# Optimization experiments

Measured on AMD Instinct MI355X. Metric: run time of the kernel, lower is better.

The kernel has to match this reference:

```python
import jax, jax.numpy as jnp
import numpy as np
import math
from math import factorial
from fractions import Fraction

LMAX = 2
N_ATOMS = 30000
N_FEAT = 128


def _cg(j1, m1, j2, m2, j3, m3):
    # Clebsch-Gordan coefficient <j1 m1 j2 m2 | j3 m3> (Racah formula, exact rationals)
    if m3 != m1 + m2 or j3 < abs(j1 - j2) or j3 > j1 + j2:
        return 0.0
    f = factorial
    pref = Fraction((2 * j3 + 1) * f(j3 + j1 - j2) * f(j3 - j1 + j2) * f(j1 + j2 - j3), f(j1 + j2 + j3 + 1))
    pref *= f(j3 + m3) * f(j3 - m3) * f(j1 - m1) * f(j1 + m1) * f(j2 - m2) * f(j2 + m2)
    s = Fraction(0)
    kmin = max(0, j2 - j3 - m1, j1 - j3 + m2)
    kmax = min(j1 + j2 - j3, j1 - m1, j2 + m2)
    for k in range(kmin, kmax + 1):
        s += Fraction((-1) ** k, f(k) * f(j1 + j2 - j3 - k) * f(j1 - m1 - k) * f(j2 + m2 - k) * f(j3 - j2 + m1 + k) * f(j3 - j1 - m2 + k))
    return math.sqrt(float(pref)) * float(s)


def _sh_indices(lmax):
    lidx = np.concatenate([np.full(2 * l + 1, l) for l in range(lmax + 1)])
    midx = np.concatenate([np.arange(-l, l + 1) for l in range(lmax + 1)])
    return lidx, midx


def _build_sparse_cg(lmax):
    # dense complex-SH CG tensor over combined (l,m) index s, size S=(lmax+1)^2
    lidx, midx = _sh_indices(lmax)
    S = len(lidx)
    cg = np.zeros((S, S, S))
    for a in range(S):
        for b in range(S):
            for c in range(S):
                cg[a, b, c] = _cg(int(lidx[a]), int(midx[a]), int(lidx[b]), int(midx[b]), int(lidx[c]), int(midx[c]))
    # unitary complex SH -> real SH transform (rows: real, cols: complex)
    m1 = midx[:, None]
    m2 = midx[None, :]
    U = ((m1 == 0) & (m2 == 0)) * (1.0 + 0.0j)
    U = U + ((m1 > 0) & (m2 > 0) & (m1 == m2)) * ((-1.0) ** m1 / math.sqrt(2))
    U = U + ((m1 > 0) & (m2 < 0) & (m1 == -m2)) * (1.0 / math.sqrt(2))
    U = U + ((m1 < 0) & (m2 > 0) & (m1 == -m2)) * (-1.0j * (-1.0) ** m1 / math.sqrt(2))
    U = U + ((m1 < 0) & (m2 < 0) & (m1 == m2)) * (1.0j / math.sqrt(2))
    U = U * (lidx[:, None] == lidx[None, :])
    cg_rsh = np.einsum('ijk,mi,nj,ok->mno', cg.astype(np.complex128), U, U, U.conj())
    # parity invariance mask
    parity = (-1.0) ** lidx
    pmask = (parity[:, None, None] * parity[None, :, None]) == parity[None, None, :]
    cg_real = (cg_rsh * pmask).real
    # sparsify (threshold kills complex-arithmetic residues ~1e-17)
    i1, i2, io = np.nonzero(np.abs(cg_real) > 1e-12)
    return cg_real[i1, i2, io].astype(np.float32), i1.astype(np.int32), i2.astype(np.int32), io.astype(np.int32)


def setup_inputs() -> dict:
    key = jax.random.key(0)
    k1, k2 = jax.random.split(key)
    S = (LMAX + 1) ** 2
    cg_sparse, i1, i2, io = _build_sparse_cg(LMAX)
    return {
        'x1': jax.random.normal(k1, (N_ATOMS, S, N_FEAT), dtype=jnp.float32),
        'x2': jax.random.normal(k2, (N_ATOMS, S, N_FEAT), dtype=jnp.float32),
        'cg_sparse': jnp.asarray(cg_sparse),
        'idx_in_1': jnp.asarray(i1),
        'idx_in_2': jnp.asarray(i2),
        'idx_out': jnp.asarray(io),
    }


def reference(x1, x2, cg_sparse, idx_in_1, idx_in_2, idx_out):
    S = (LMAX + 1) ** 2
    # gather paths [n_atoms, P, F], multiply by sparse CG, scatter-add over output (l,m)
    y = x1[:, idx_in_1, :] * x2[:, idx_in_2, :] * cg_sparse[None, :, None]
    out = jnp.zeros((x1.shape[0], S, x1.shape[2]), x1.dtype).at[:, idx_out, :].add(y)
    return out
```

## Files before the change

### kernel.cpp

```cpp
#include <hip/hip_runtime.h>


#define NS 9
#define NF 128
#define NF4 32

constexpr int LQ[9] = {0, 1, 1, 1, 2, 2, 2, 2, 2};
constexpr int MQ[9] = {0, -1, 0, 1, -2, -1, 0, 1, 2};

constexpr bool cg_compat(int A, int B, int O) {
  const int l1 = LQ[A], l2 = LQ[B], l3 = LQ[O];
  const int m1 = MQ[A], m2 = MQ[B], m3 = MQ[O];
  const int lo = (l1 > l2) ? (l1 - l2) : (l2 - l1);
  if (l3 < lo || l3 > l1 + l2) return false;
  if ((l1 + l2 + l3) & 1) return false;
  const int u = (m1 < 0) ? -m1 : m1;
  const int v = (m2 < 0) ? -m2 : m2;
  const int w = (m3 < 0) ? -m3 : m3;
  const int d = (u > v) ? (u - v) : (v - u);
  if (!(w == u + v || w == d)) return false;
  const bool mixed = (m1 < 0) != (m2 < 0);
  if (mixed != (m3 < 0)) return false;
  return true;
}

__global__ void build_dense_cg(const float* __restrict__ cg,
                               const int* __restrict__ i1,
                               const int* __restrict__ i2,
                               const int* __restrict__ io,
                               int nnz, float* __restrict__ C) {
  const int t = threadIdx.x;
  for (int i = t; i < NS * NS * NS; i += blockDim.x) C[i] = 0.0f;
  __syncthreads();
  for (int k = t; k < nnz; k += blockDim.x) {
    C[(i1[k] * NS + i2[k]) * NS + io[k]] = cg[k];
  }
}

__global__ __launch_bounds__(256) void so3_tp_kernel(
    const float4* __restrict__ x1, const float4* __restrict__ x2,
    const float* __restrict__ C, float4* __restrict__ out, int total) {
  const int tid = blockIdx.x * 256 + threadIdx.x;
  if (tid >= total) return;
  const int atom = tid >> 5;
  const int f4 = tid & 31;

  const float4* ap = x1 + (size_t)atom * NS * NF4 + f4;
  const float4* bp = x2 + (size_t)atom * NS * NF4 + f4;

  float4 a[NS], b[NS];
#pragma unroll
  for (int s = 0; s < NS; s++) {
    a[s] = ap[s * NF4];
    b[s] = bp[s * NF4];
  }

  float4 acc[NS];
#pragma unroll
  for (int s = 0; s < NS; s++) acc[s] = make_float4(0.f, 0.f, 0.f, 0.f);

#pragma unroll
  for (int ia = 0; ia < NS; ia++) {
#pragma unroll
    for (int ib = 0; ib < NS; ib++) {
      const float tx = a[ia].x * b[ib].x;
      const float ty = a[ia].y * b[ib].y;
      const float tz = a[ia].z * b[ib].z;
      const float tw = a[ia].w * b[ib].w;
#pragma unroll
      for (int o = 0; o < NS; o++) {
        if (cg_compat(ia, ib, o)) {
          const float c = C[(ia * NS + ib) * NS + o];
          acc[o].x = fmaf(c, tx, acc[o].x);
          acc[o].y = fmaf(c, ty, acc[o].y);
          acc[o].z = fmaf(c, tz, acc[o].z);
          acc[o].w = fmaf(c, tw, acc[o].w);
        }
      }
    }
  }

  float4* op = out + (size_t)atom * NS * NF4 + f4;
#pragma unroll
  for (int s = 0; s < NS; s++) op[s * NF4] = acc[s];
}

extern "C" void kernel_launch(void* const* d_in, const int* in_sizes, int n_in,
                              void* d_out, int out_size, void* d_ws, size_t ws_size,
                              hipStream_t stream) {
  const float* x1 = (const float*)d_in[0];
  const float* x2 = (const float*)d_in[1];
  const float* cg = (const float*)d_in[2];
  const int* i1 = (const int*)d_in[3];
  const int* i2 = (const int*)d_in[4];
  const int* io = (const int*)d_in[5];

  const int nnz = in_sizes[2];
  const int natoms = in_sizes[0] / (NS * NF);
  float* C = (float*)d_ws;

  build_dense_cg<<<1, 256, 0, stream>>>(cg, i1, i2, io, nnz, C);

  const int total = natoms * NF4;
  const int blocks = (total + 255) / 256;
  so3_tp_kernel<<<blocks, 256, 0, stream>>>((const float4*)x1, (const float4*)x2, C,
                                            (float4*)d_out, total);
}
```

Measured before the change: 329.8 us.

## Reorder tensor product loops output-major with nontemporal stores and occupancy hint

Restructures the contraction so each output component is accumulated in one float4 and stored right away, instead of keeping nine accumulators live. The dense CG table is rebuilt output-major so the per-output coefficient reads are contiguous. The change also adds a launch-bounds occupancy hint of 4, uses 32-bit index math, and writes outputs with nontemporal stores to cut register pressure and cache pollution. In exchange, the a*b products are recomputed per output instead of shared across outputs, adding multiplies to a kernel that is likely memory-bound.

```diff
diff --git a/kernel.cpp b/kernel.cpp
--- a/kernel.cpp
+++ b/kernel.cpp
@@ -4,6 +4,8 @@
 #define NS 9
 #define NF 128
 #define NF4 32
+
+typedef float vf4 __attribute__((ext_vector_type(4)));
 
 constexpr int LQ[9] = {0, 1, 1, 1, 2, 2, 2, 2, 2};
 constexpr int MQ[9] = {0, -1, 0, 1, -2, -1, 0, 1, 2};
@@ -33,56 +35,47 @@
   for (int i = t; i < NS * NS * NS; i += blockDim.x) C[i] = 0.0f;
   __syncthreads();
   for (int k = t; k < nnz; k += blockDim.x) {
-    C[(i1[k] * NS + i2[k]) * NS + io[k]] = cg[k];
+    C[io[k] * (NS * NS) + i1[k] * NS + i2[k]] = cg[k];
   }
 }
 
-__global__ __launch_bounds__(256) void so3_tp_kernel(
+__global__ __launch_bounds__(256, 4) void so3_tp_kernel(
     const float4* __restrict__ x1, const float4* __restrict__ x2,
     const float* __restrict__ C, float4* __restrict__ out, int total) {
   const int tid = blockIdx.x * 256 + threadIdx.x;
   if (tid >= total) return;
   const int atom = tid >> 5;
   const int f4 = tid & 31;
+  const int base = atom * (NS * NF4) + f4;
 
-  const float4* ap = x1 + (size_t)atom * NS * NF4 + f4;
-  const float4* bp = x2 + (size_t)atom * NS * NF4 + f4;
+  const float4* ap = x1 + base;
+  const float4* bp = x2 + base;
 
   float4 a[NS], b[NS];
 #pragma unroll
-  for (int s = 0; s < NS; s++) {
-    a[s] = ap[s * NF4];
-    b[s] = bp[s * NF4];
-  }
+  for (int s = 0; s < NS; s++) a[s] = ap[s * NF4];
+#pragma unroll
+  for (int s = 0; s < NS; s++) b[s] = bp[s * NF4];
 
-  float4 acc[NS];
+  float4* op = out + base;
 #pragma unroll
-  for (int s = 0; s < NS; s++) acc[s] = make_float4(0.f, 0.f, 0.f, 0.f);
-
+  for (int o = 0; o < NS; o++) {
+    float4 acc = make_float4(0.f, 0.f, 0.f, 0.f);
 #pragma unroll
-  for (int ia = 0; ia < NS; ia++) {
+    for (int ia = 0; ia < NS; ia++) {
 #pragma unroll
-    for (int ib = 0; ib < NS; ib++) {
-      const float tx = a[ia].x * b[ib].x;
-      const float ty = a[ia].y * b[ib].y;
-      const float tz = a[ia].z * b[ib].z;
-      const float tw = a[ia].w * b[ib].w;
-#pragma unroll
-      for (int o = 0; o < NS; o++) {
+      for (int ib = 0; ib < NS; ib++) {
         if (cg_compat(ia, ib, o)) {
-          const float c = C[(ia * NS + ib) * NS + o];
-          acc[o].x = fmaf(c, tx, acc[o].x);
-          acc[o].y = fmaf(c, ty, acc[o].y);
-          acc[o].z = fmaf(c, tz, acc[o].z);
-          acc[o].w = fmaf(c, tw, acc[o].w);
+          const float c = C[o * (NS * NS) + ia * NS + ib];
+          acc.x = fmaf(c, a[ia].x * b[ib].x, acc.x);
+          acc.y = fmaf(c, a[ia].y * b[ib].y, acc.y);
+          acc.z = fmaf(c, a[ia].z * b[ib].z, acc.z);
+          acc.w = fmaf(c, a[ia].w * b[ib].w, acc.w);
         }
       }
     }
+    __builtin_nontemporal_store(*(const vf4*)&acc, (vf4*)(op + o * NF4));
   }
-
-  float4* op = out + (size_t)atom * NS * NF4 + f4;
-#pragma unroll
-  for (int s = 0; s < NS; s++) op[s * NF4] = acc[s];
 }
 
 extern "C" void kernel_launch(void* const* d_in, const int* in_sizes, int n_in,
```

Measured after the change: 341.4 us. +3.5%, slower.
